# Optimization experiments

Hardware: AMD Instinct MI355X
Metric: run time of the kernel (lower is better)

The kernel has to match this reference:

```python
import jax, jax.numpy as jnp
import numpy as np
import math

B = 4096
D = 768
HID = 256
C_OLD = 100
C_NEW = 100
NUM_CLASSES = 200
EPSILON = 0.05
TAU = 0.1
EPS = 1e-8
NEG_INF = -1e9


def _l2_normalize(x):
    # matches F.normalize(p=2, dim=1, eps=1e-12)
    n = jnp.linalg.norm(x, axis=1, keepdims=True)
    return x / jnp.maximum(n, 1e-12)


def setup_inputs() -> dict:
    key = jax.random.key(0)
    k1, k2, k3, k4, k5, k6, k7 = jax.random.split(key, 7)
    z_u = jax.random.normal(k1, (B, D), dtype=jnp.float32)
    logits = jax.random.normal(k2, (B, NUM_CLASSES), dtype=jnp.float32)
    old_class_indices = jnp.arange(C_OLD, dtype=jnp.int64 if jax.config.jax_enable_x64 else jnp.int32)
    new_class_indices = jnp.arange(C_OLD, C_OLD + C_NEW, dtype=old_class_indices.dtype)
    base_features = jax.random.normal(k3, (B, D), dtype=jnp.float32)
    s = 1.0 / math.sqrt(D)
    f1_w = jax.random.uniform(k4, (HID, D), dtype=jnp.float32, minval=-s, maxval=s)
    f1_b = jax.random.uniform(k5, (HID,), dtype=jnp.float32, minval=-s, maxval=s)
    f2_w = jax.random.uniform(k6, (HID, D), dtype=jnp.float32, minval=-s, maxval=s)
    f2_b = jax.random.uniform(k7, (HID,), dtype=jnp.float32, minval=-s, maxval=s)
    return {"z_u": z_u, "logits": logits, "old_class_indices": old_class_indices,
            "new_class_indices": new_class_indices, "base_features": base_features,
            "f1_w": f1_w, "f1_b": f1_b, "f2_w": f2_w, "f2_b": f2_b}


def reference(z_u, logits, old_class_indices, new_class_indices, base_features,
              f1_w, f1_b, f2_w, f2_b):
    num_old = old_class_indices.shape[0]
    active = jnp.concatenate([old_class_indices, new_class_indices])

    # ---- soft entropy regularization ----
    probs = jax.nn.softmax(logits[:, active], axis=1)   # (B, C_old+C_new)
    mean_probs = probs.mean(axis=0)
    p_old = mean_probs[:num_old].sum()
    p_new = mean_probs[num_old:].sum()
    loss_inter = (p_old * jnp.log(p_old + EPS) + p_new * jnp.log(p_new + EPS)
                  + math.log(2.0))
    p_old_in = mean_probs[:num_old] / (p_old + EPS)
    loss_old_in = jnp.sum(p_old_in * jnp.log(p_old_in + EPS)) + math.log(num_old)
    p_new_in = mean_probs[num_old:] / (p_new + EPS)
    num_new = new_class_indices.shape[0]
    if num_new > 1:
        loss_new_in = jnp.sum(p_new_in * jnp.log(p_new_in + EPS)) + math.log(num_new)
    else:
        loss_new_in = jnp.float32(0.0)
    loss_entropy = loss_inter + loss_old_in + loss_new_in

    # ---- neighborhood mask from frozen base features ----
    base_norm = _l2_normalize(base_features)
    base_sim = base_norm @ base_norm.T                  # (B, B)
    eye = jnp.eye(base_sim.shape[0], dtype=bool)
    mask = (base_sim > EPSILON) & ~eye                  # (B, B) bool

    # ---- contrastive similarities ----
    z_norm = _l2_normalize(z_u)
    sim = z_norm @ z_norm.T                             # (B, B)

    f1_z = z_u @ f1_w.T + f1_b                          # (B, HID)
    f2_z = z_u @ f2_w.T + f2_b
    attn_logits = jnp.where(mask, f1_z @ f2_z.T, NEG_INF)
    w_ik = jax.nn.softmax(attn_logits, axis=1) * mask.astype(sim.dtype)

    exp_sim = jnp.where(eye, 0.0, jnp.exp(sim / TAU))
    denom = exp_sim.sum(axis=1, keepdims=True)
    log_prob = sim / TAU - jnp.log(denom + EPS)

    num_neighbors = mask.sum(axis=1).astype(sim.dtype)  # (B,)
    valid = num_neighbors > 0
    loss_i = -(w_ik * mask.astype(sim.dtype) * log_prob).sum(axis=1)
    per_sample = jnp.where(valid, loss_i / jnp.maximum(num_neighbors, 1.0), 0.0)
    n_valid = valid.sum().astype(sim.dtype)
    loss_contrastive = jnp.where(n_valid > 0,
                                 per_sample.sum() / jnp.maximum(n_valid, 1.0),
                                 0.0)

    total_loss = loss_entropy + loss_contrastive
    return total_loss
```

## Files before the change

kernel.cpp:

```cpp
#include <hip/hip_runtime.h>
#include <hip/hip_fp8.h>


#define B_N   4096
#define D_N   768
#define HID_N 256
#define NCLS  200

typedef __attribute__((ext_vector_type(8))) short v8s;
typedef __attribute__((ext_vector_type(4))) float v4f;

__device__ __forceinline__ unsigned short f2bf(float x) {
    unsigned int u = __float_as_uint(x);
    unsigned int r = (u + 0x7FFFu + ((u >> 16) & 1u)) >> 16;
    return (unsigned short)r;
}
__device__ __forceinline__ float bf2f(unsigned short h) {
    return __uint_as_float((unsigned int)h << 16);
}
__device__ __forceinline__ unsigned char f2fp8(float x) {
    __hip_fp8_e4m3 v(x);
    return (unsigned char)v.__x;
}

__device__ __forceinline__ void gld16c(const unsigned char* g, unsigned char* l) {
    __builtin_amdgcn_global_load_lds(
        (__attribute__((address_space(1))) void*)g,
        (__attribute__((address_space(3))) void*)l, 16, 0, 0);
}

#define ZERO_ACC(a) { _Pragma("unroll") for (int _i = 0; _i < 4; _i++) \
    _Pragma("unroll") for (int _j = 0; _j < 4; _j++) a[_i][_j] = (v4f){0.f,0.f,0.f,0.f}; }

__global__ __launch_bounds__(256) void pre_all(
    const float* __restrict__ z, const float* __restrict__ base,
    const float* __restrict__ w1, const float* __restrict__ w2,
    const float* __restrict__ b1, const float* __restrict__ b2,
    const float* __restrict__ logits, const int* __restrict__ oldi,
    const int* __restrict__ newi,
    unsigned char* __restrict__ zn8, unsigned char* __restrict__ bn8,
    unsigned char* __restrict__ f1z8, unsigned char* __restrict__ f2z8,
    float* __restrict__ mpart, float* __restrict__ accums)
{
    __shared__ __align__(16) unsigned char shmem[2 * 64 * 72 * 2];
    int tid = threadIdx.x;

    if (blockIdx.x < B_N) {
        float* ws1 = (float*)shmem;
        float* ws2 = ws1 + 4;
        int row = blockIdx.x;
        const float* zr = z    + (size_t)row * D_N;
        const float* br = base + (size_t)row * D_N;
        float z0 = zr[tid], z1 = zr[tid + 256], z2 = zr[tid + 512];
        float b0 = br[tid], b1v = br[tid + 256], b2v = br[tid + 512];
        float s1 = z0*z0 + z1*z1 + z2*z2;
        float s2 = b0*b0 + b1v*b1v + b2v*b2v;
        #pragma unroll
        for (int m = 32; m > 0; m >>= 1) { s1 += __shfl_xor(s1, m); s2 += __shfl_xor(s2, m); }
        if ((tid & 63) == 0) { ws1[tid >> 6] = s1; ws2[tid >> 6] = s2; }
        __syncthreads();
        float t1 = ws1[0] + ws1[1] + ws1[2] + ws1[3];
        float t2 = ws2[0] + ws2[1] + ws2[2] + ws2[3];
        float sc1 = 16.0f / fmaxf(sqrtf(t1), 1e-12f);
        float sc2 = 16.0f / fmaxf(sqrtf(t2), 1e-12f);
        size_t o = (size_t)row * D_N;
        int j0 = tid ^ (((row >> 3) & 1) << 3);
        zn8[o+j0] = f2fp8(z0*sc1);  zn8[o+j0+256] = f2fp8(z1*sc1);  zn8[o+j0+512] = f2fp8(z2*sc1);
        bn8[o+j0] = f2fp8(b0*sc2);  bn8[o+j0+256] = f2fp8(b1v*sc2); bn8[o+j0+512] = f2fp8(b2v*sc2);
        return;
    }
    if (blockIdx.x < B_N + 256) {
        int* act = (int*)shmem;
        float* accs = (float*)(shmem + 1024);
        int sb = blockIdx.x - B_N;
        int lane = tid & 63, wave = tid >> 6;
        if (sb == 0 && tid < 4) accums[tid] = 0.0f;
        if (tid < NCLS) act[tid] = (tid < 100) ? oldi[tid] : newi[tid - 100];
        accs[tid] = 0.f; accs[256 + tid] = 0.f; accs[512 + tid] = 0.f; accs[768 + tid] = 0.f;
        __syncthreads();
        int a0 = act[lane], a1 = act[lane + 64], a2 = act[lane + 128];
        int a3 = (lane < 8) ? act[lane + 192] : 0;
        int r0 = sb * 16 + wave * 4;
        float c0 = 0.f, c1 = 0.f, c2 = 0.f, c3 = 0.f;
        for (int i = 0; i < 4; i++) {
            const float* lr = logits + (size_t)(r0 + i) * NCLS;
            float x0 = lr[a0], x1 = lr[a1], x2 = lr[a2];
            float x3 = (lane < 8) ? lr[a3] : -3.0e38f;
            float m = fmaxf(fmaxf(x0, x1), fmaxf(x2, x3));
            #pragma unroll
            for (int s = 32; s > 0; s >>= 1) m = fmaxf(m, __shfl_xor(m, s));
            float e0 = __expf(x0 - m), e1 = __expf(x1 - m), e2 = __expf(x2 - m);
            float e3 = (lane < 8) ? __expf(x3 - m) : 0.f;
            float sm = e0 + e1 + e2 + e3;
            #pragma unroll
            for (int s = 32; s > 0; s >>= 1) sm += __shfl_xor(sm, s);
            float inv = 1.0f / sm;
            c0 += e0 * inv; c1 += e1 * inv; c2 += e2 * inv; c3 += e3 * inv;
        }
        accs[wave * 256 + lane] = c0; accs[wave * 256 + lane + 64] = c1;
        accs[wave * 256 + lane + 128] = c2;
        if (lane < 8) accs[wave * 256 + lane + 192] = c3;
        __syncthreads();
        mpart[(size_t)tid * 256 + sb] =
            accs[tid] + accs[256 + tid] + accs[512 + tid] + accs[768 + tid];
        return;
    }
    {
        unsigned short* Al = (unsigned short*)shmem;
        unsigned short* Bl = Al + 64 * 72;
        int f = blockIdx.x - (B_N + 256);
        int which = f >> 8;
        int t6 = f & 255;
        int mBase = (t6 >> 2) * 64;
        int nBase = (t6 & 3) * 64;
        const float* wsrc = which ? w2 : w1;
        const float* bias = which ? b2 : b1;
        unsigned char* outz = which ? f2z8 : f1z8;
        int lane = tid & 63, wave = tid >> 6, quad = lane >> 4, col = lane & 15;
        v4f acc[4];
        #pragma unroll
        for (int i = 0; i < 4; i++) acc[i] = (v4f){0.f, 0.f, 0.f, 0.f};
        for (int kc = 0; kc < D_N; kc += 64) {
            __syncthreads();
            #pragma unroll
            for (int s = 0; s < 4; s++) {
                int slot = s * 256 + tid;
                int row = slot >> 4, k4 = slot & 15;
                float4 va = *(const float4*)(z + (size_t)(mBase + row) * D_N + kc + k4 * 4);
                float4 vb = *(const float4*)(wsrc + (size_t)(nBase + row) * D_N + kc + k4 * 4);
                unsigned short* pa = Al + row * 72 + k4 * 4;
                unsigned short* pb = Bl + row * 72 + k4 * 4;
                pa[0] = f2bf(va.x); pa[1] = f2bf(va.y); pa[2] = f2bf(va.z); pa[3] = f2bf(va.w);
                pb[0] = f2bf(vb.x); pb[1] = f2bf(vb.y); pb[2] = f2bf(vb.z); pb[3] = f2bf(vb.w);
            }
            __syncthreads();
            #pragma unroll
            for (int kk = 0; kk < 2; kk++) {
                v8s af = *(const v8s*)(Al + (wave * 16 + col) * 72 + kk * 32 + quad * 8);
                #pragma unroll
                for (int tc = 0; tc < 4; tc++) {
                    v8s bf = *(const v8s*)(Bl + (tc * 16 + col) * 72 + kk * 32 + quad * 8);
                    acc[tc] = __builtin_amdgcn_mfma_f32_16x16x32_bf16(af, bf, acc[tc], 0, 0, 0);
                }
            }
        }
        #pragma unroll
        for (int tc = 0; tc < 4; tc++) {
            int gcol = nBase + tc * 16 + col;
            float bv = bias[gcol];
            #pragma unroll
            for (int reg = 0; reg < 4; reg++) {
                int grow = mBase + wave * 16 + quad * 4 + reg;
                int sw8 = ((grow >> 3) & 1) << 3;
                outz[(size_t)grow * HID_N + (gcol ^ sw8)] =
                    f2fp8(4.0f * (acc[tc][reg] + bv));
            }
        }
    }
}

__global__ __launch_bounds__(256, 2) void main_fused(
    const unsigned char* __restrict__ zn8, const unsigned char* __restrict__ bn8,
    const unsigned char* __restrict__ f1z8, const unsigned char* __restrict__ f2z8,
    float* __restrict__ partials)
{
    __shared__ __align__(16) unsigned char S[4 * 128 * 128];
    unsigned char* S0 = S;
    unsigned char* S1 = S + 1 * 128 * 128;
    unsigned char* S2 = S + 2 * 128 * 128;
    unsigned char* S3 = S + 3 * 128 * 128;
    int tid = threadIdx.x, lane = tid & 63, wave = tid >> 6, quad = lane >> 4, col = lane & 15;
    int wr = wave >> 1, wc = wave & 1;
    int ib = blockIdx.x, jc = blockIdx.y;
    int rBase = ib * 128 + wr * 64;
    int cBase = jc * 128 + wc * 64;
    const int r8 = lane >> 3;
    const int kbl8 = (lane & 7) ^ r8;
    const int sub8 = ((quad & 1) ^ (col >> 3)) << 3;

    v4f accB[4][4], accS[4][4];
    ZERO_ACC(accB); ZERO_ACC(accS);
    for (int kc = 0; kc < D_N; kc += 128) {
        __syncthreads();
        #pragma unroll
        for (int s = 0; s < 4; s++) {
            int rowbase = s * 32 + wave * 8;
            size_t rOff = (size_t)(ib * 128 + rowbase + r8) * D_N + kc + kbl8 * 16;
            size_t cOff = (size_t)(jc * 128 + rowbase + r8) * D_N + kc + kbl8 * 16;
            gld16c(bn8 + rOff, S0 + rowbase * 128);
            gld16c(bn8 + cOff, S1 + rowbase * 128);
            gld16c(zn8 + rOff, S2 + rowbase * 128);
            gld16c(zn8 + cOff, S3 + rowbase * 128);
        }
        __syncthreads();
        #pragma unroll
        for (int kk = 0; kk < 4; kk++) {
            int gbase = kk * 2 + (quad >> 1);
            int off = ((gbase ^ (col & 7)) << 4) + sub8;
            long a1[4], b1[4], a2[4], b2[4];
            #pragma unroll
            for (int t = 0; t < 4; t++) {
                int rA = (wr * 64 + t * 16 + col) * 128;
                int rB = (wc * 64 + t * 16 + col) * 128;
                a1[t] = *(const long*)(S0 + rA + off);
                b1[t] = *(const long*)(S1 + rB + off);
                a2[t] = *(const long*)(S2 + rA + off);
                b2[t] = *(const long*)(S3 + rB + off);
            }
            #pragma unroll
            for (int tr = 0; tr < 4; tr++)
                #pragma unroll
                for (int tc = 0; tc < 4; tc++) {
                    accB[tr][tc] = __builtin_amdgcn_mfma_f32_16x16x32_fp8_fp8(
                        a1[tr], b1[tc], accB[tr][tc], 0, 0, 0);
                    accS[tr][tc] = __builtin_amdgcn_mfma_f32_16x16x32_fp8_fp8(
                        a2[tr], b2[tc], accS[tr][tc], 0, 0, 0);
                }
        }
    }

    unsigned char* F1 = S0;
    unsigned char* F2 = S0 + 32768;
    __syncthreads();
    {
        int r4 = lane >> 4;
        #pragma unroll
        for (int s = 0; s < 8; s++) {
            int rowbase = s * 16 + wave * 4;
            int row = rowbase + r4;
            int kb = (lane & 15) ^ (row & 15);
            gld16c(f1z8 + (size_t)(ib * 128 + row) * HID_N + kb * 16, F1 + rowbase * 256);
            gld16c(f2z8 + (size_t)(jc * 128 + row) * HID_N + kb * 16, F2 + rowbase * 256);
        }
    }

    unsigned long long mb = 0ull;
    #pragma unroll
    for (int tr = 0; tr < 4; tr++)
        #pragma unroll
        for (int tc = 0; tc < 4; tc++)
            #pragma unroll
            for (int reg = 0; reg < 4; reg++) {
                int grow = rBase + tr * 16 + quad * 4 + reg;
                int gcol = cBase + tc * 16 + col;
                if (accB[tr][tc][reg] > 12.8f && grow != gcol)
                    mb |= 1ull << (tr * 16 + tc * 4 + reg);
            }

    float dsum[16];
    #pragma unroll
    for (int i = 0; i < 16; i++) dsum[i] = 0.f;
    unsigned int svp[4][4][2];
    #pragma unroll
    for (int tr = 0; tr < 4; tr++)
        #pragma unroll
        for (int tc = 0; tc < 4; tc++) {
            float s0 = accS[tr][tc][0] * 0.00390625f;
            float s1 = accS[tr][tc][1] * 0.00390625f;
            float s2 = accS[tr][tc][2] * 0.00390625f;
            float s3 = accS[tr][tc][3] * 0.00390625f;
            float svv[4] = {s0, s1, s2, s3};
            #pragma unroll
            for (int reg = 0; reg < 4; reg++) {
                int grow = rBase + tr * 16 + quad * 4 + reg;
                int gcol = cBase + tc * 16 + col;
                if (grow != gcol) dsum[tr * 4 + reg] += __expf(svv[reg] * 10.0f);
            }
            svp[tr][tc][0] = ((unsigned int)f2bf(s1) << 16) | f2bf(s0);
            svp[tr][tc][1] = ((unsigned int)f2bf(s3) << 16) | f2bf(s2);
        }

    v4f accA[4][4]; ZERO_ACC(accA);
    __syncthreads();
    #pragma unroll
    for (int kk = 0; kk < 8; kk++) {
        int gbase = kk * 2 + (quad >> 1);
        int off = ((gbase ^ col) << 4) + sub8;
        long af[4], bf[4];
        #pragma unroll
        for (int t = 0; t < 4; t++) {
            af[t] = *(const long*)(F1 + (wr * 64 + t * 16 + col) * 256 + off);
            bf[t] = *(const long*)(F2 + (wc * 64 + t * 16 + col) * 256 + off);
        }
        #pragma unroll
        for (int tr = 0; tr < 4; tr++)
            #pragma unroll
            for (int tc = 0; tc < 4; tc++)
                accA[tr][tc] = __builtin_amdgcn_mfma_f32_16x16x32_fp8_fp8(
                    af[tr], bf[tc], accA[tr][tc], 0, 0, 0);
    }

    float lsum[16], asum[16], nnf[16];
    #pragma unroll
    for (int i = 0; i < 16; i++) { lsum[i] = 0.f; asum[i] = 0.f; nnf[i] = 0.f; }
    #pragma unroll
    for (int tr = 0; tr < 4; tr++)
        #pragma unroll
        for (int tc = 0; tc < 4; tc++)
            #pragma unroll
            for (int reg = 0; reg < 4; reg++) {
                if ((mb >> (tr * 16 + tc * 4 + reg)) & 1ull) {
                    int slot = tr * 4 + reg;
                    float e = __expf(accA[tr][tc][reg] * 0.0625f);
                    unsigned int pk = svp[tr][tc][reg >> 1];
                    float sv = bf2f((unsigned short)((reg & 1) ? (pk >> 16) : (pk & 0xFFFF)));
                    lsum[slot] += e;
                    asum[slot] += e * sv;
                    nnf[slot] += 1.f;
                }
            }

    #pragma unroll
    for (int i = 0; i < 16; i++) {
        #pragma unroll
        for (int m = 1; m < 16; m <<= 1) {
            lsum[i] += __shfl_xor(lsum[i], m);
            asum[i] += __shfl_xor(asum[i], m);
            dsum[i] += __shfl_xor(dsum[i], m);
            nnf[i]  += __shfl_xor(nnf[i], m);
        }
        if (col == 0) {
            int row = rBase + (i >> 2) * 16 + quad * 4 + (i & 3);
            float4 v; v.x = lsum[i]; v.y = asum[i]; v.z = dsum[i]; v.w = nnf[i];
            *(float4*)(partials + ((size_t)row * 64 + jc * 2 + wc) * 4) = v;
        }
    }
}

__global__ __launch_bounds__(256) void row_reduce_fin(
    const float* __restrict__ partials, const float* __restrict__ mpart,
    float* __restrict__ acc, float* __restrict__ out)
{
    int tid = threadIdx.x;
    int row = blockIdx.x * 64 + (tid >> 2);
    int sub = tid & 3;
    const float4* p = (const float4*)partials + (size_t)row * 64 + sub * 16;
    float L = 0.f, A = 0.f, Dn = 0.f, NN = 0.f;
    #pragma unroll
    for (int c = 0; c < 16; c++) { float4 v = p[c]; L += v.x; A += v.y; Dn += v.z; NN += v.w; }
    #pragma unroll
    for (int m = 1; m < 4; m <<= 1) {
        L += __shfl_xor(L, m); A += __shfl_xor(A, m);
        Dn += __shfl_xor(Dn, m); NN += __shfl_xor(NN, m);
    }
    float per = 0.f, val = 0.f;
    if (sub == 0 && NN > 0.5f) {
        per = (logf(Dn + 1e-8f) - 10.0f * (A / L)) / NN;
        val = 1.0f;
    }
    __shared__ float red[256];
    __shared__ float r2s[256];
    __shared__ int amLast;
    red[tid] = per; r2s[tid] = val; __syncthreads();
    for (int s = 128; s > 0; s >>= 1) {
        if (tid < s) { red[tid] += red[tid + s]; r2s[tid] += r2s[tid + s]; }
        __syncthreads();
    }
    if (tid == 0) {
        atomicAdd(&acc[0], red[0]);
        atomicAdd(&acc[1], r2s[0]);
        __threadfence();
        int old = atomicAdd((int*)&acc[2], 1);
        amLast = (old == (int)gridDim.x - 1);
    }
    __syncthreads();
    if (!amLast) return;

    __shared__ float bcast[2];
    float pcl = 0.0f;
    if (tid < NCLS) {
        const float4* mp = (const float4*)(mpart + (size_t)tid * 256);
        float s = 0.f;
        #pragma unroll
        for (int c = 0; c < 64; c++) { float4 v = mp[c]; s += v.x + v.y + v.z + v.w; }
        pcl = s * (1.0f / 4096.0f);
    }
    red[tid] = (tid < 100) ? pcl : 0.0f; __syncthreads();
    for (int s = 128; s > 0; s >>= 1) { if (tid < s) red[tid] += red[tid + s]; __syncthreads(); }
    if (tid == 0) bcast[0] = red[0];
    __syncthreads();
    red[tid] = (tid >= 100 && tid < NCLS) ? pcl : 0.0f; __syncthreads();
    for (int s = 128; s > 0; s >>= 1) { if (tid < s) red[tid] += red[tid + s]; __syncthreads(); }
    if (tid == 0) bcast[1] = red[0];
    __syncthreads();
    float p_old = bcast[0], p_new = bcast[1];

    float t = 0.0f;
    if (tid < 100)       { float q = pcl / (p_old + 1e-8f); t = q * logf(q + 1e-8f); }
    else if (tid < NCLS) { float q = pcl / (p_new + 1e-8f); t = q * logf(q + 1e-8f); }
    red[tid] = t; __syncthreads();
    for (int s = 128; s > 0; s >>= 1) { if (tid < s) red[tid] += red[tid + s]; __syncthreads(); }

    if (tid == 0) {
        float s0 = __hip_atomic_load(&acc[0], __ATOMIC_RELAXED, __HIP_MEMORY_SCOPE_AGENT);
        float s1 = __hip_atomic_load(&acc[1], __ATOMIC_RELAXED, __HIP_MEMORY_SCOPE_AGENT);
        float loss_inter = p_old * logf(p_old + 1e-8f) + p_new * logf(p_new + 1e-8f)
                           + 0.69314718056f;
        float loss_entropy = loss_inter + red[0] + 2.0f * 4.60517018599f;
        float lc = (s1 > 0.5f) ? s0 / s1 : 0.0f;
        out[0] = loss_entropy + lc;
    }
}

extern "C" void kernel_launch(void* const* d_in, const int* in_sizes, int n_in,
                              void* d_out, int out_size, void* d_ws, size_t ws_size,
                              hipStream_t stream)
{
    const float* z_u    = (const float*)d_in[0];
    const float* logits = (const float*)d_in[1];
    const int*   oldi   = (const int*)d_in[2];
    const int*   newi   = (const int*)d_in[3];
    const float* basef  = (const float*)d_in[4];
    const float* f1w    = (const float*)d_in[5];
    const float* f1b    = (const float*)d_in[6];
    const float* f2w    = (const float*)d_in[7];
    const float* f2b    = (const float*)d_in[8];
    float* out = (float*)d_out;

    unsigned char* zn8   = (unsigned char*)d_ws;
    unsigned char* bn8   = zn8 + (size_t)B_N * D_N;
    unsigned char* f1z8  = bn8 + (size_t)B_N * D_N;
    unsigned char* f2z8  = f1z8 + (size_t)B_N * HID_N;
    float* partials = (float*)(f2z8 + (size_t)B_N * HID_N);
    float* mpart    = partials + (size_t)B_N * 64 * 4;
    float* accums   = mpart + 256 * 256;

    pre_all<<<B_N + 256 + 512, 256, 0, stream>>>(
        z_u, basef, f1w, f2w, f1b, f2b, logits, oldi, newi,
        zn8, bn8, f1z8, f2z8, mpart, accums);
    main_fused<<<dim3(32, 32), 256, 0, stream>>>(zn8, bn8, f1z8, f2z8, partials);
    row_reduce_fin<<<64, 256, 0, stream>>>(partials, mpart, accums, out);
}
```

Before: 172.1 us.

## Exploit symmetry of base and z similarity matrices to compute only upper-triangle tiles

```diff
diff --git a/kernel.cpp b/kernel.cpp
--- a/kernel.cpp
+++ b/kernel.cpp
@@ -171,13 +171,29 @@
     unsigned char* S3 = S + 3 * 128 * 128;
     int tid = threadIdx.x, lane = tid & 63, wave = tid >> 6, quad = lane >> 4, col = lane & 15;
     int wr = wave >> 1, wc = wave & 1;
-    int ib = blockIdx.x, jc = blockIdx.y;
+
+    int bid = blockIdx.x;
+    int ib, jc;
+    if (bid < 496) {
+        int p = bid;
+        int t = (int)((1.0f + sqrtf(8.0f * (float)p + 1.0f)) * 0.5f);
+        while (t * (t - 1) / 2 > p) --t;
+        while ((t + 1) * t / 2 <= p) ++t;
+        jc = t; ib = p - t * (t - 1) / 2;
+    } else {
+        ib = jc = bid - 496;
+    }
+    const bool offd = (ib != jc);
+
     int rBase = ib * 128 + wr * 64;
     int cBase = jc * 128 + wc * 64;
     const int r8 = lane >> 3;
     const int kbl8 = (lane & 7) ^ r8;
     const int sub8 = ((quad & 1) ^ (col >> 3)) << 3;
 
+    const unsigned char* S1r = offd ? S1 : S0;
+    const unsigned char* S3r = offd ? S3 : S2;
+
     v4f accB[4][4], accS[4][4];
     ZERO_ACC(accB); ZERO_ACC(accS);
     for (int kc = 0; kc < D_N; kc += 128) {
@@ -186,11 +202,13 @@
         for (int s = 0; s < 4; s++) {
             int rowbase = s * 32 + wave * 8;
             size_t rOff = (size_t)(ib * 128 + rowbase + r8) * D_N + kc + kbl8 * 16;
-            size_t cOff = (size_t)(jc * 128 + rowbase + r8) * D_N + kc + kbl8 * 16;
             gld16c(bn8 + rOff, S0 + rowbase * 128);
-            gld16c(bn8 + cOff, S1 + rowbase * 128);
             gld16c(zn8 + rOff, S2 + rowbase * 128);
-            gld16c(zn8 + cOff, S3 + rowbase * 128);
+            if (offd) {
+                size_t cOff = (size_t)(jc * 128 + rowbase + r8) * D_N + kc + kbl8 * 16;
+                gld16c(bn8 + cOff, S1 + rowbase * 128);
+                gld16c(zn8 + cOff, S3 + rowbase * 128);
+            }
         }
         __syncthreads();
         #pragma unroll
@@ -203,9 +221,9 @@
                 int rA = (wr * 64 + t * 16 + col) * 128;
                 int rB = (wc * 64 + t * 16 + col) * 128;
                 a1[t] = *(const long*)(S0 + rA + off);
-                b1[t] = *(const long*)(S1 + rB + off);
+                b1[t] = *(const long*)(S1r + rB + off);
                 a2[t] = *(const long*)(S2 + rA + off);
-                b2[t] = *(const long*)(S3 + rB + off);
+                b2[t] = *(const long*)(S3r + rB + off);
             }
             #pragma unroll
             for (int tr = 0; tr < 4; tr++)
@@ -243,13 +261,15 @@
             for (int reg = 0; reg < 4; reg++) {
                 int grow = rBase + tr * 16 + quad * 4 + reg;
                 int gcol = cBase + tc * 16 + col;
-                if (accB[tr][tc][reg] > 12.8f && grow != gcol)
+                if (accB[tr][tc][reg] > 12.8f && (offd || grow != gcol))
                     mb |= 1ull << (tr * 16 + tc * 4 + reg);
             }
 
-    float dsum[16];
+    float dsum[16], d2[4];
     #pragma unroll
     for (int i = 0; i < 16; i++) dsum[i] = 0.f;
+    #pragma unroll
+    for (int i = 0; i < 4; i++) d2[i] = 0.f;
     unsigned int svp[4][4][2];
     #pragma unroll
     for (int tr = 0; tr < 4; tr++)
@@ -262,9 +282,15 @@
             float svv[4] = {s0, s1, s2, s3};
             #pragma unroll
             for (int reg = 0; reg < 4; reg++) {
-                int grow = rBase + tr * 16 + quad * 4 + reg;
-                int gcol = cBase + tc * 16 + col;
-                if (grow != gcol) dsum[tr * 4 + reg] += __expf(svv[reg] * 10.0f);
+                float e = __expf(svv[reg] * 10.0f);
+                if (offd) {
+                    dsum[tr * 4 + reg] += e;
+                    d2[tc] += e;
+                } else {
+                    int grow = rBase + tr * 16 + quad * 4 + reg;
+                    int gcol = cBase + tc * 16 + col;
+                    if (grow != gcol) dsum[tr * 4 + reg] += e;
+                }
             }
             svp[tr][tc][0] = ((unsigned int)f2bf(s1) << 16) | f2bf(s0);
             svp[tr][tc][1] = ((unsigned int)f2bf(s3) << 16) | f2bf(s2);
@@ -290,39 +316,108 @@
                     af[tr], bf[tc], accA[tr][tc], 0, 0, 0);
     }
 
-    float lsum[16], asum[16], nnf[16];
-    #pragma unroll
-    for (int i = 0; i < 16; i++) { lsum[i] = 0.f; asum[i] = 0.f; nnf[i] = 0.f; }
-    #pragma unroll
-    for (int tr = 0; tr < 4; tr++)
-        #pragma unroll
-        for (int tc = 0; tc < 4; tc++)
-            #pragma unroll
-            for (int reg = 0; reg < 4; reg++) {
-                if ((mb >> (tr * 16 + tc * 4 + reg)) & 1ull) {
-                    int slot = tr * 4 + reg;
-                    float e = __expf(accA[tr][tc][reg] * 0.0625f);
-                    unsigned int pk = svp[tr][tc][reg >> 1];
-                    float sv = bf2f((unsigned short)((reg & 1) ? (pk >> 16) : (pk & 0xFFFF)));
-                    lsum[slot] += e;
-                    asum[slot] += e * sv;
-                    nnf[slot] += 1.f;
+    __syncthreads();
+    if (offd) {
+        int r4 = lane >> 4;
+        #pragma unroll
+        for (int s = 0; s < 8; s++) {
+            int rowbase = s * 16 + wave * 4;
+            int row = rowbase + r4;
+            int kb = (lane & 15) ^ (row & 15);
+            gld16c(f2z8 + (size_t)(ib * 128 + row) * HID_N + kb * 16, F1 + rowbase * 256);
+            gld16c(f1z8 + (size_t)(jc * 128 + row) * HID_N + kb * 16, F2 + rowbase * 256);
+        }
+    }
+
+    {
+        float lsum[16], asum[16], nnf[16];
+        #pragma unroll
+        for (int i = 0; i < 16; i++) { lsum[i] = 0.f; asum[i] = 0.f; nnf[i] = 0.f; }
+        #pragma unroll
+        for (int tr = 0; tr < 4; tr++)
+            #pragma unroll
+            for (int tc = 0; tc < 4; tc++)
+                #pragma unroll
+                for (int reg = 0; reg < 4; reg++) {
+                    if ((mb >> (tr * 16 + tc * 4 + reg)) & 1ull) {
+                        int slot = tr * 4 + reg;
+                        float e = __expf(accA[tr][tc][reg] * 0.0625f);
+                        unsigned int pk = svp[tr][tc][reg >> 1];
+                        float sv = bf2f((unsigned short)((reg & 1) ? (pk >> 16) : (pk & 0xFFFF)));
+                        lsum[slot] += e;
+                        asum[slot] += e * sv;
+                        nnf[slot] += 1.f;
+                    }
                 }
-            }
-
-    #pragma unroll
-    for (int i = 0; i < 16; i++) {
-        #pragma unroll
-        for (int m = 1; m < 16; m <<= 1) {
-            lsum[i] += __shfl_xor(lsum[i], m);
-            asum[i] += __shfl_xor(asum[i], m);
-            dsum[i] += __shfl_xor(dsum[i], m);
-            nnf[i]  += __shfl_xor(nnf[i], m);
-        }
-        if (col == 0) {
-            int row = rBase + (i >> 2) * 16 + quad * 4 + (i & 3);
-            float4 v; v.x = lsum[i]; v.y = asum[i]; v.z = dsum[i]; v.w = nnf[i];
-            *(float4*)(partials + ((size_t)row * 64 + jc * 2 + wc) * 4) = v;
+        #pragma unroll
+        for (int i = 0; i < 16; i++) {
+            #pragma unroll
+            for (int m = 1; m < 16; m <<= 1) {
+                lsum[i] += __shfl_xor(lsum[i], m);
+                asum[i] += __shfl_xor(asum[i], m);
+                dsum[i] += __shfl_xor(dsum[i], m);
+                nnf[i]  += __shfl_xor(nnf[i], m);
+            }
+            if (col == 0) {
+                int row = rBase + (i >> 2) * 16 + quad * 4 + (i & 3);
+                float4 v; v.x = lsum[i]; v.y = asum[i]; v.z = dsum[i]; v.w = nnf[i];
+                *(float4*)(partials + ((size_t)row * 64 + jc * 2 + wc) * 4) = v;
+            }
+        }
+    }
+
+    if (offd) {
+        ZERO_ACC(accA);
+        __syncthreads();
+        #pragma unroll
+        for (int kk = 0; kk < 8; kk++) {
+            int gbase = kk * 2 + (quad >> 1);
+            int off = ((gbase ^ col) << 4) + sub8;
+            long af[4], bf[4];
+            #pragma unroll
+            for (int t = 0; t < 4; t++) {
+                af[t] = *(const long*)(F1 + (wr * 64 + t * 16 + col) * 256 + off);
+                bf[t] = *(const long*)(F2 + (wc * 64 + t * 16 + col) * 256 + off);
+            }
+            #pragma unroll
+            for (int tr = 0; tr < 4; tr++)
+                #pragma unroll
+                for (int tc = 0; tc < 4; tc++)
+                    accA[tr][tc] = __builtin_amdgcn_mfma_f32_16x16x32_fp8_fp8(
+                        af[tr], bf[tc], accA[tr][tc], 0, 0, 0);
+        }
+        float l2[4], a2[4], n2[4];
+        #pragma unroll
+        for (int i = 0; i < 4; i++) { l2[i] = 0.f; a2[i] = 0.f; n2[i] = 0.f; }
+        #pragma unroll
+        for (int tr = 0; tr < 4; tr++)
+            #pragma unroll
+            for (int tc = 0; tc < 4; tc++)
+                #pragma unroll
+                for (int reg = 0; reg < 4; reg++) {
+                    if ((mb >> (tr * 16 + tc * 4 + reg)) & 1ull) {
+                        float e = __expf(accA[tr][tc][reg] * 0.0625f);
+                        unsigned int pk = svp[tr][tc][reg >> 1];
+                        float sv = bf2f((unsigned short)((reg & 1) ? (pk >> 16) : (pk & 0xFFFF)));
+                        l2[tc] += e;
+                        a2[tc] += e * sv;
+                        n2[tc] += 1.f;
+                    }
+                }
+        #pragma unroll
+        for (int tc = 0; tc < 4; tc++) {
+            #pragma unroll
+            for (int m = 16; m < 64; m <<= 1) {
+                l2[tc] += __shfl_xor(l2[tc], m);
+                a2[tc] += __shfl_xor(a2[tc], m);
+                d2[tc] += __shfl_xor(d2[tc], m);
+                n2[tc] += __shfl_xor(n2[tc], m);
+            }
+            if (quad == 0) {
+                int row = cBase + tc * 16 + col;
+                float4 v; v.x = l2[tc]; v.y = a2[tc]; v.z = d2[tc]; v.w = n2[tc];
+                *(float4*)(partials + ((size_t)row * 64 + ib * 2 + wr) * 4) = v;
+            }
         }
     }
 }
@@ -428,6 +523,6 @@
     pre_all<<<B_N + 256 + 512, 256, 0, stream>>>(
         z_u, basef, f1w, f2w, f1b, f2b, logits, oldi, newi,
         zn8, bn8, f1z8, f2z8, mpart, accums);
-    main_fused<<<dim3(32, 32), 256, 0, stream>>>(zn8, bn8, f1z8, f2z8, partials);
+    main_fused<<<496 + 32, 256, 0, stream>>>(zn8, bn8, f1z8, f2z8, partials);
     row_reduce_fin<<<64, 256, 0, stream>>>(partials, mpart, accums, out);
 }
```

Result: slower. 203.2 us (+18.1%).

## Reorder pre_all blocks, normalize rows per-wave with vectorized fp8 stores

Applied to the files above, without the earlier changes.

```diff
diff --git a/kernel.cpp b/kernel.cpp
--- a/kernel.cpp
+++ b/kernel.cpp
@@ -8,6 +8,7 @@
 #define NCLS  200
 
 typedef __attribute__((ext_vector_type(8))) short v8s;
+typedef __attribute__((ext_vector_type(4))) short v4ss;
 typedef __attribute__((ext_vector_type(4))) float v4f;
 
 __device__ __forceinline__ unsigned short f2bf(float x) {
@@ -21,6 +22,10 @@
 __device__ __forceinline__ unsigned char f2fp8(float x) {
     __hip_fp8_e4m3 v(x);
     return (unsigned char)v.__x;
+}
+__device__ __forceinline__ unsigned int pack4fp8(float a, float b, float c, float d) {
+    return (unsigned int)f2fp8(a) | ((unsigned int)f2fp8(b) << 8) |
+           ((unsigned int)f2fp8(c) << 16) | ((unsigned int)f2fp8(d) << 24);
 }
 
 __device__ __forceinline__ void gld16c(const unsigned char* g, unsigned char* l) {
@@ -45,34 +50,66 @@
     __shared__ __align__(16) unsigned char shmem[2 * 64 * 72 * 2];
     int tid = threadIdx.x;
 
-    if (blockIdx.x < B_N) {
-        float* ws1 = (float*)shmem;
-        float* ws2 = ws1 + 4;
-        int row = blockIdx.x;
-        const float* zr = z    + (size_t)row * D_N;
-        const float* br = base + (size_t)row * D_N;
-        float z0 = zr[tid], z1 = zr[tid + 256], z2 = zr[tid + 512];
-        float b0 = br[tid], b1v = br[tid + 256], b2v = br[tid + 512];
-        float s1 = z0*z0 + z1*z1 + z2*z2;
-        float s2 = b0*b0 + b1v*b1v + b2v*b2v;
-        #pragma unroll
-        for (int m = 32; m > 0; m >>= 1) { s1 += __shfl_xor(s1, m); s2 += __shfl_xor(s2, m); }
-        if ((tid & 63) == 0) { ws1[tid >> 6] = s1; ws2[tid >> 6] = s2; }
-        __syncthreads();
-        float t1 = ws1[0] + ws1[1] + ws1[2] + ws1[3];
-        float t2 = ws2[0] + ws2[1] + ws2[2] + ws2[3];
-        float sc1 = 16.0f / fmaxf(sqrtf(t1), 1e-12f);
-        float sc2 = 16.0f / fmaxf(sqrtf(t2), 1e-12f);
-        size_t o = (size_t)row * D_N;
-        int j0 = tid ^ (((row >> 3) & 1) << 3);
-        zn8[o+j0] = f2fp8(z0*sc1);  zn8[o+j0+256] = f2fp8(z1*sc1);  zn8[o+j0+512] = f2fp8(z2*sc1);
-        bn8[o+j0] = f2fp8(b0*sc2);  bn8[o+j0+256] = f2fp8(b1v*sc2); bn8[o+j0+512] = f2fp8(b2v*sc2);
+    if (blockIdx.x < 512) {
+        unsigned short* Al = (unsigned short*)shmem;
+        unsigned short* Bl = Al + 64 * 72;
+        int f = blockIdx.x;
+        int which = f >> 8;
+        int t6 = f & 255;
+        int mBase = (t6 >> 2) * 64;
+        int nBase = (t6 & 3) * 64;
+        const float* wsrc = which ? w2 : w1;
+        const float* bias = which ? b2 : b1;
+        unsigned char* outz = which ? f2z8 : f1z8;
+        int lane = tid & 63, wave = tid >> 6, quad = lane >> 4, col = lane & 15;
+        v4f acc[4];
+        #pragma unroll
+        for (int i = 0; i < 4; i++) acc[i] = (v4f){0.f, 0.f, 0.f, 0.f};
+        for (int kc = 0; kc < D_N; kc += 64) {
+            __syncthreads();
+            #pragma unroll
+            for (int s = 0; s < 4; s++) {
+                int slot = s * 256 + tid;
+                int row = slot >> 4, k4 = slot & 15;
+                float4 va = *(const float4*)(z + (size_t)(mBase + row) * D_N + kc + k4 * 4);
+                float4 vb = *(const float4*)(wsrc + (size_t)(nBase + row) * D_N + kc + k4 * 4);
+                v4ss sa, sb;
+                sa[0] = (short)f2bf(va.x); sa[1] = (short)f2bf(va.y);
+                sa[2] = (short)f2bf(va.z); sa[3] = (short)f2bf(va.w);
+                sb[0] = (short)f2bf(vb.x); sb[1] = (short)f2bf(vb.y);
+                sb[2] = (short)f2bf(vb.z); sb[3] = (short)f2bf(vb.w);
+                *(v4ss*)(Al + row * 72 + k4 * 4) = sa;
+                *(v4ss*)(Bl + row * 72 + k4 * 4) = sb;
+            }
+            __syncthreads();
+            #pragma unroll
+            for (int kk = 0; kk < 2; kk++) {
+                v8s af = *(const v8s*)(Al + (wave * 16 + col) * 72 + kk * 32 + quad * 8);
+                #pragma unroll
+                for (int tc = 0; tc < 4; tc++) {
+                    v8s bf = *(const v8s*)(Bl + (tc * 16 + col) * 72 + kk * 32 + quad * 8);
+                    acc[tc] = __builtin_amdgcn_mfma_f32_16x16x32_bf16(af, bf, acc[tc], 0, 0, 0);
+                }
+            }
+        }
+        #pragma unroll
+        for (int tc = 0; tc < 4; tc++) {
+            int gcol = nBase + tc * 16 + col;
+            float bv = bias[gcol];
+            #pragma unroll
+            for (int reg = 0; reg < 4; reg++) {
+                int grow = mBase + wave * 16 + quad * 4 + reg;
+                int sw8 = ((grow >> 3) & 1) << 3;
+                outz[(size_t)grow * HID_N + (gcol ^ sw8)] =
+                    f2fp8(4.0f * (acc[tc][reg] + bv));
+            }
+        }
         return;
     }
-    if (blockIdx.x < B_N + 256) {
+    if (blockIdx.x < 768) {
         int* act = (int*)shmem;
         float* accs = (float*)(shmem + 1024);
-        int sb = blockIdx.x - B_N;
+        int sb = blockIdx.x - 512;
         int lane = tid & 63, wave = tid >> 6;
         if (sb == 0 && tid < 4) accums[tid] = 0.0f;
         if (tid < NCLS) act[tid] = (tid < 100) ? oldi[tid] : newi[tid - 100];
@@ -106,55 +143,46 @@
         return;
     }
     {
-        unsigned short* Al = (unsigned short*)shmem;
-        unsigned short* Bl = Al + 64 * 72;
-        int f = blockIdx.x - (B_N + 256);
-        int which = f >> 8;
-        int t6 = f & 255;
-        int mBase = (t6 >> 2) * 64;
-        int nBase = (t6 & 3) * 64;
-        const float* wsrc = which ? w2 : w1;
-        const float* bias = which ? b2 : b1;
-        unsigned char* outz = which ? f2z8 : f1z8;
-        int lane = tid & 63, wave = tid >> 6, quad = lane >> 4, col = lane & 15;
-        v4f acc[4];
-        #pragma unroll
-        for (int i = 0; i < 4; i++) acc[i] = (v4f){0.f, 0.f, 0.f, 0.f};
-        for (int kc = 0; kc < D_N; kc += 64) {
-            __syncthreads();
-            #pragma unroll
-            for (int s = 0; s < 4; s++) {
-                int slot = s * 256 + tid;
-                int row = slot >> 4, k4 = slot & 15;
-                float4 va = *(const float4*)(z + (size_t)(mBase + row) * D_N + kc + k4 * 4);
-                float4 vb = *(const float4*)(wsrc + (size_t)(nBase + row) * D_N + kc + k4 * 4);
-                unsigned short* pa = Al + row * 72 + k4 * 4;
-                unsigned short* pb = Bl + row * 72 + k4 * 4;
-                pa[0] = f2bf(va.x); pa[1] = f2bf(va.y); pa[2] = f2bf(va.z); pa[3] = f2bf(va.w);
-                pb[0] = f2bf(vb.x); pb[1] = f2bf(vb.y); pb[2] = f2bf(vb.z); pb[3] = f2bf(vb.w);
-            }
-            __syncthreads();
-            #pragma unroll
-            for (int kk = 0; kk < 2; kk++) {
-                v8s af = *(const v8s*)(Al + (wave * 16 + col) * 72 + kk * 32 + quad * 8);
-                #pragma unroll
-                for (int tc = 0; tc < 4; tc++) {
-                    v8s bf = *(const v8s*)(Bl + (tc * 16 + col) * 72 + kk * 32 + quad * 8);
-                    acc[tc] = __builtin_amdgcn_mfma_f32_16x16x32_bf16(af, bf, acc[tc], 0, 0, 0);
-                }
-            }
-        }
-        #pragma unroll
-        for (int tc = 0; tc < 4; tc++) {
-            int gcol = nBase + tc * 16 + col;
-            float bv = bias[gcol];
-            #pragma unroll
-            for (int reg = 0; reg < 4; reg++) {
-                int grow = mBase + wave * 16 + quad * 4 + reg;
-                int sw8 = ((grow >> 3) & 1) << 3;
-                outz[(size_t)grow * HID_N + (gcol ^ sw8)] =
-                    f2fp8(4.0f * (acc[tc][reg] + bv));
-            }
+        int nb = blockIdx.x - 768;
+        int lane = tid & 63, wave = tid >> 6;
+        #pragma unroll
+        for (int rr = 0; rr < 2; rr++) {
+            int row = nb * 8 + rr * 4 + wave;
+            const float* zr = z    + (size_t)row * D_N;
+            const float* br = base + (size_t)row * D_N;
+            float4 zv0 = *(const float4*)(zr + (size_t)lane * 4);
+            float4 zv1 = *(const float4*)(zr + (size_t)(lane + 64) * 4);
+            float4 zv2 = *(const float4*)(zr + (size_t)(lane + 128) * 4);
+            float4 bv0 = *(const float4*)(br + (size_t)lane * 4);
+            float4 bv1 = *(const float4*)(br + (size_t)(lane + 64) * 4);
+            float4 bv2 = *(const float4*)(br + (size_t)(lane + 128) * 4);
+            float s1 = zv0.x*zv0.x + zv0.y*zv0.y + zv0.z*zv0.z + zv0.w*zv0.w
+                     + zv1.x*zv1.x + zv1.y*zv1.y + zv1.z*zv1.z + zv1.w*zv1.w
+                     + zv2.x*zv2.x + zv2.y*zv2.y + zv2.z*zv2.z + zv2.w*zv2.w;
+            float s2 = bv0.x*bv0.x + bv0.y*bv0.y + bv0.z*bv0.z + bv0.w*bv0.w
+                     + bv1.x*bv1.x + bv1.y*bv1.y + bv1.z*bv1.z + bv1.w*bv1.w
+                     + bv2.x*bv2.x + bv2.y*bv2.y + bv2.z*bv2.z + bv2.w*bv2.w;
+            #pragma unroll
+            for (int m = 32; m > 0; m >>= 1) {
+                s1 += __shfl_xor(s1, m);
+                s2 += __shfl_xor(s2, m);
+            }
+            float sc1 = 16.0f / fmaxf(sqrtf(s1), 1e-12f);
+            float sc2 = 16.0f / fmaxf(sqrtf(s2), 1e-12f);
+            size_t o = (size_t)row * D_N;
+            int sw8 = ((row >> 3) & 1) << 3;
+            *(unsigned int*)(zn8 + o + (((lane      ) * 4) ^ sw8)) =
+                pack4fp8(zv0.x*sc1, zv0.y*sc1, zv0.z*sc1, zv0.w*sc1);
+            *(unsigned int*)(zn8 + o + (((lane +  64) * 4) ^ sw8)) =
+                pack4fp8(zv1.x*sc1, zv1.y*sc1, zv1.z*sc1, zv1.w*sc1);
+            *(unsigned int*)(zn8 + o + (((lane + 128) * 4) ^ sw8)) =
+                pack4fp8(zv2.x*sc1, zv2.y*sc1, zv2.z*sc1, zv2.w*sc1);
+            *(unsigned int*)(bn8 + o + (((lane      ) * 4) ^ sw8)) =
+                pack4fp8(bv0.x*sc2, bv0.y*sc2, bv0.z*sc2, bv0.w*sc2);
+            *(unsigned int*)(bn8 + o + (((lane +  64) * 4) ^ sw8)) =
+                pack4fp8(bv1.x*sc2, bv1.y*sc2, bv1.z*sc2, bv1.w*sc2);
+            *(unsigned int*)(bn8 + o + (((lane + 128) * 4) ^ sw8)) =
+                pack4fp8(bv2.x*sc2, bv2.y*sc2, bv2.z*sc2, bv2.w*sc2);
         }
     }
 }
@@ -425,7 +453,7 @@
     float* mpart    = partials + (size_t)B_N * 64 * 4;
     float* accums   = mpart + 256 * 256;
 
-    pre_all<<<B_N + 256 + 512, 256, 0, stream>>>(
+    pre_all<<<512 + 256 + 512, 256, 0, stream>>>(
         z_u, basef, f1w, f2w, f1b, f2b, logits, oldi, newi,
         zn8, bn8, f1z8, f2z8, mpart, accums);
     main_fused<<<dim3(32, 32), 256, 0, stream>>>(zn8, bn8, f1z8, f2z8, partials);
```

New measurement: 169.5 us. About the same (-1.5%).
